# Kernel tuning notes

Measured on AMD Instinct MI355X. Metric: run time of the kernel, lower is better.

## Reference

```python
import jax, jax.numpy as jnp
import numpy as np
import math

B, S, H = 2, 2048, 1024
NH, HD = 16, 64
MAX_SCALE = 4


def setup_inputs() -> dict:
    key = jax.random.key(0)
    ks = jax.random.split(key, 8)
    s = 0.02
    return {
        "x": jax.random.normal(ks[0], (B, S, H), dtype=jnp.float32),
        "Wqkv": jax.random.normal(ks[1], (H, 3 * H), dtype=jnp.float32) * s,
        "bqkv": jnp.zeros((3 * H,), dtype=jnp.float32),
        "Wout": jax.random.normal(ks[2], (H, H), dtype=jnp.float32) * s,
        "bout": jnp.zeros((H,), dtype=jnp.float32),
        "Wscale": jax.random.normal(ks[3], (H, MAX_SCALE), dtype=jnp.float32) * s,
        "bscale": jnp.zeros((MAX_SCALE,), dtype=jnp.float32),
    }


def reference(x, Wqkv, bqkv, Wout, bout, Wscale, bscale):
    b, s, h = x.shape
    inv_sqrt_hd = 1.0 / math.sqrt(HD)
    # qkv projection -> [3, b, nh, s, hd]
    qkv = (x @ Wqkv + bqkv).reshape(b, s, 3, NH, HD).transpose(2, 0, 3, 1, 4)
    q, k, v = qkv[0], qkv[1], qkv[2]
    # per-token soft weights over scales [b, s, max_scale]
    scale_weights = jax.nn.softmax(x @ Wscale + bscale, axis=-1)
    out = jnp.zeros((b, NH, s, HD), dtype=x.dtype)
    for scale_idx in range(MAX_SCALE):
        dilation = 2 ** scale_idx
        kd = k[:, :, ::dilation]  # strided (dilated) gather of keys
        vd = v[:, :, ::dilation]
        scores = jnp.einsum("bhqd,bhkd->bhqk", q, kd) * inv_sqrt_hd
        attn = jax.nn.softmax(scores, axis=-1)
        o = jnp.einsum("bhqk,bhkd->bhqd", attn, vd)
        w = scale_weights[:, :, scale_idx][:, None, :, None]  # [b,1,s,1]
        out = out + o * w
    out = out.transpose(0, 2, 1, 3).reshape(b, s, h)
    return out @ Wout + bout
```

## Files before the change

kernel.cpp:

```cpp
#include <hip/hip_runtime.h>
#include <stdint.h>

typedef unsigned short u16;
typedef __attribute__((ext_vector_type(8))) __bf16 bf8v;
typedef __attribute__((ext_vector_type(4))) float f4v;
typedef __attribute__((ext_vector_type(16))) float f16v;

#define BB 2
#define SS 2048
#define HH 1024

#define OFF_Q   0u
#define OFF_K0  8388608u
#define OFF_K1  16777216u
#define OFF_K2  20971520u
#define OFF_K3  23068672u
#define OFF_V0  24117248u
#define OFF_V1  32505856u
#define OFF_V2  36700160u
#define OFF_V3  38797312u
#define OFF_WQT 39845888u
#define OFF_WOT 46137344u
#define OFF_XB  48234496u
#define OFF_SCW 56623104u

__device__ __forceinline__ u16 f2bf(float f) {
    union { float f; uint32_t u; } v; v.f = f;
    uint32_t r = v.u + 0x7fffu + ((v.u >> 16) & 1u);
    return (u16)(r >> 16);
}
__device__ __forceinline__ uint32_t pk2(float a, float b) {
    return (uint32_t)f2bf(a) | ((uint32_t)f2bf(b) << 16);
}
__device__ __forceinline__ uint32_t pkt2(float a, float b) {
    union { float f; uint32_t u; } x, y; x.f = a; y.f = b;
    return (x.u >> 16) | (y.u & 0xffff0000u);
}

__global__ __launch_bounds__(256) void xconv_kernel(const float* __restrict__ x,
                                                    u16* __restrict__ xb) {
    size_t t = (size_t)blockIdx.x * 256 + threadIdx.x;
    float4 v = *(const float4*)&x[t * 4];
    uint2 pk; pk.x = pk2(v.x, v.y); pk.y = pk2(v.z, v.w);
    *(uint2*)&xb[t * 4] = pk;
}

__global__ __launch_bounds__(256) void wconv_kernel(const float* __restrict__ W,
                                                    u16* __restrict__ Wt,
                                                    int N, int K) {
    __shared__ float tile[64][69];
    const int tid = threadIdx.x;
    const int n0 = blockIdx.x * 64, k0 = blockIdx.y * 64;
    const int r = tid >> 4, c4 = (tid & 15) * 4;
#pragma unroll
    for (int it = 0; it < 4; it++) {
        float4 v = *(const float4*)&W[(size_t)(k0 + it * 16 + r) * N + n0 + c4];
        tile[it * 16 + r][c4 + 0] = v.x; tile[it * 16 + r][c4 + 1] = v.y;
        tile[it * 16 + r][c4 + 2] = v.z; tile[it * 16 + r][c4 + 3] = v.w;
    }
    __syncthreads();
#pragma unroll
    for (int it = 0; it < 4; it++) {
        int n = it * 16 + r;
        uint2 pk;
        pk.x = pk2(tile[c4 + 0][n], tile[c4 + 1][n]);
        pk.y = pk2(tile[c4 + 2][n], tile[c4 + 3][n]);
        *(uint2*)&Wt[(size_t)(n0 + n) * K + k0 + c4] = pk;
    }
}

__global__ __launch_bounds__(256) void scale_kernel(const float* __restrict__ x,
                                                    const float* __restrict__ Wscale,
                                                    const float* __restrict__ bscale,
                                                    float* __restrict__ scw) {
    const int lane = threadIdx.x & 63;
    const int wid  = threadIdx.x >> 6;
    const int row  = blockIdx.x * 4 + wid;
    float a0 = 0.f, a1 = 0.f, a2 = 0.f, a3 = 0.f;
    for (int i = 0; i < 16; i++) {
        int hh = lane + i * 64;
        float xs = x[(size_t)row * HH + hh];
        float4 wv = *(const float4*)&Wscale[hh * 4];
        a0 += xs * wv.x; a1 += xs * wv.y; a2 += xs * wv.z; a3 += xs * wv.w;
    }
    for (int off = 1; off < 64; off <<= 1) {
        a0 += __shfl_xor(a0, off); a1 += __shfl_xor(a1, off);
        a2 += __shfl_xor(a2, off); a3 += __shfl_xor(a3, off);
    }
    if (lane == 0) {
        a0 += bscale[0]; a1 += bscale[1]; a2 += bscale[2]; a3 += bscale[3];
        float mx = fmaxf(fmaxf(a0, a1), fmaxf(a2, a3));
        float e0 = __expf(a0 - mx), e1 = __expf(a1 - mx);
        float e2 = __expf(a2 - mx), e3 = __expf(a3 - mx);
        float inv = 1.f / (e0 + e1 + e2 + e3);
        float4 o = {e0 * inv, e1 * inv, e2 * inv, e3 * inv};
        *(float4*)&scw[(size_t)row * 4] = o;
    }
}

template<int MODE>
__global__ __launch_bounds__(256) void gemm_bt(const u16* __restrict__ A,
                                               const u16* __restrict__ Bt,
                                               const float* __restrict__ bias,
                                               void* __restrict__ Cp,
                                               int N, int K) {
    __shared__ __align__(16) u16 At[128 * 40];
    __shared__ __align__(16) u16 Btl[128 * 40];
    const int tid  = threadIdx.x;
    const int lane = tid & 63;
    const int wid  = tid >> 6;
    const int l15  = lane & 15;
    const int quad = lane >> 4;
    const int wm = wid & 1, wn = wid >> 1;
    const int m0 = blockIdx.y * 128;
    const int n0 = blockIdx.x * 128;
    const int srow = tid >> 2;
    const int sc8  = (tid & 3) * 8;

    f4v acc[4][4];
#pragma unroll
    for (int i = 0; i < 4; i++)
#pragma unroll
        for (int j = 0; j < 4; j++) acc[i][j] = (f4v){0.f, 0.f, 0.f, 0.f};

    uint4 pa0 = *(const uint4*)(A  + (size_t)(m0 + srow) * K + sc8);
    uint4 pa1 = *(const uint4*)(A  + (size_t)(m0 + srow + 64) * K + sc8);
    uint4 pb0 = *(const uint4*)(Bt + (size_t)(n0 + srow) * K + sc8);
    uint4 pb1 = *(const uint4*)(Bt + (size_t)(n0 + srow + 64) * K + sc8);

    for (int kc = 0; kc < K; kc += 32) {
        __syncthreads();
        *(uint4*)&At[srow * 40 + sc8]         = pa0;
        *(uint4*)&At[(srow + 64) * 40 + sc8]  = pa1;
        *(uint4*)&Btl[srow * 40 + sc8]        = pb0;
        *(uint4*)&Btl[(srow + 64) * 40 + sc8] = pb1;
        __syncthreads();
        if (kc + 32 < K) {
            pa0 = *(const uint4*)(A  + (size_t)(m0 + srow) * K + kc + 32 + sc8);
            pa1 = *(const uint4*)(A  + (size_t)(m0 + srow + 64) * K + kc + 32 + sc8);
            pb0 = *(const uint4*)(Bt + (size_t)(n0 + srow) * K + kc + 32 + sc8);
            pb1 = *(const uint4*)(Bt + (size_t)(n0 + srow + 64) * K + kc + 32 + sc8);
        }
        bf8v af[4], bf[4];
#pragma unroll
        for (int t = 0; t < 4; t++) {
            af[t] = *(const bf8v*)&At[(wm * 64 + t * 16 + l15) * 40 + quad * 8];
            bf[t] = *(const bf8v*)&Btl[(wn * 64 + t * 16 + l15) * 40 + quad * 8];
        }
#pragma unroll
        for (int ti = 0; ti < 4; ti++)
#pragma unroll
            for (int tj = 0; tj < 4; tj++)
                acc[ti][tj] = __builtin_amdgcn_mfma_f32_16x16x32_bf16(af[ti], bf[tj], acc[ti][tj], 0, 0, 0);
    }

    if (MODE == 0) {
#pragma unroll
        for (int ti = 0; ti < 4; ti++)
#pragma unroll
            for (int tj = 0; tj < 4; tj++)
#pragma unroll
                for (int r = 0; r < 4; r++) {
                    int m = m0 + wm * 64 + ti * 16 + quad * 4 + r;
                    int n = n0 + wn * 64 + tj * 16 + l15;
                    ((float*)Cp)[(size_t)m * N + n] = acc[ti][tj][r] + bias[n];
                }
    } else {
        char* ws = (char*)Cp;
        u16* Qd = (u16*)ws;
        u16* K0 = (u16*)(ws + OFF_K0); u16* K1 = (u16*)(ws + OFF_K1);
        u16* K2 = (u16*)(ws + OFF_K2); u16* K3 = (u16*)(ws + OFF_K3);
        u16* V0 = (u16*)(ws + OFF_V0); u16* V1 = (u16*)(ws + OFF_V1);
        u16* V2 = (u16*)(ws + OFF_V2); u16* V3 = (u16*)(ws + OFF_V3);
        const int region = n0 >> 10;
        if (region == 0) {
#pragma unroll
            for (int ti = 0; ti < 4; ti++)
#pragma unroll
                for (int tj = 0; tj < 4; tj++)
#pragma unroll
                    for (int r = 0; r < 4; r++) {
                        int m = m0 + wm * 64 + ti * 16 + quad * 4 + r;
                        int n = n0 + wn * 64 + tj * 16 + l15;
                        Qd[(size_t)m * 1024 + n] = f2bf(acc[ti][tj][r] + bias[n]);
                    }
        } else if (region == 1) {
#pragma unroll
            for (int ti = 0; ti < 4; ti++)
#pragma unroll
                for (int tj = 0; tj < 4; tj++) {
                    int n  = n0 + wn * 64 + tj * 16 + l15;
                    int nk = n - 1024;
                    int h = nk >> 6, hd = nk & 63;
#pragma unroll
                    for (int r = 0; r < 4; r++) {
                        int m = m0 + wm * 64 + ti * 16 + quad * 4 + r;
                        int bb = m >> 11, tok = m & 2047;
                        int bh = bb * 16 + h;
                        u16 bv = f2bf((acc[ti][tj][r] + bias[n]) * 0.125f);
                        K0[((size_t)bh * 2048 + tok) * 64 + hd] = bv;
                        if (!(r & 1)) K1[((size_t)bh * 1024 + (tok >> 1)) * 64 + hd] = bv;
                        if (r == 0) {
                            K2[((size_t)bh * 512 + (tok >> 2)) * 64 + hd] = bv;
                            if (!(quad & 1)) K3[((size_t)bh * 256 + (tok >> 3)) * 64 + hd] = bv;
                        }
                    }
                }
        } else {
#pragma unroll
            for (int ti = 0; ti < 4; ti++)
#pragma unroll
                for (int tj = 0; tj < 4; tj++) {
                    int n  = n0 + wn * 64 + tj * 16 + l15;
                    int nv = n - 2048;
                    int h = nv >> 6, hd = nv & 63;
                    int tokb = m0 + wm * 64 + ti * 16 + quad * 4;
                    int bb = tokb >> 11, tok = tokb & 2047;
                    int bh = bb * 16 + h;
                    float v0 = acc[ti][tj][0] + bias[n];
                    float v1 = acc[ti][tj][1] + bias[n];
                    float v2 = acc[ti][tj][2] + bias[n];
                    float v3 = acc[ti][tj][3] + bias[n];
                    u16 c0 = f2bf(v0), c1 = f2bf(v1), c2 = f2bf(v2), c3 = f2bf(v3);
                    uint2 pk;
                    pk.x = (uint32_t)c0 | ((uint32_t)c1 << 16);
                    pk.y = (uint32_t)c2 | ((uint32_t)c3 << 16);
                    *(uint2*)&V0[((size_t)bh * 64 + hd) * 2048 + tok] = pk;
                    *(uint32_t*)&V1[((size_t)bh * 64 + hd) * 1024 + (tok >> 1)] =
                        (uint32_t)c0 | ((uint32_t)c2 << 16);
                    V2[((size_t)bh * 64 + hd) * 512 + (tok >> 2)] = c0;
                    if (!(quad & 1)) V3[((size_t)bh * 64 + hd) * 256 + (tok >> 3)] = c0;
                }
        }
    }
}

__global__ void attn_kernel(const char* __restrict__ ws) {
    __shared__ __align__(16) u16 smem[14848];
    u16* Kt0 = smem;
    u16* Kt1 = smem + 2304;
    u16* Vt0 = smem + 4608;
    u16* Vt1 = smem + 7168;
    u16* Pt  = smem + 9728;

    const u16* Qd    = (const u16*)(ws + OFF_Q);
    const float* scw = (const float*)(ws + OFF_SCW);
    u16* attnb       = (u16*)(ws + OFF_Q);

    const int tid  = threadIdx.x;
    const int lane = tid & 63;
    const int wid  = tid >> 6;
    const int l31  = lane & 31;
    const int half = lane >> 5;
    const int b = blockIdx.z, h = blockIdx.y;
    const int q  = blockIdx.x * 128 + wid * 32 + l31;
    const int bh = b * 16 + h;

    const int skey = tid >> 3;
    const int shd8 = (tid & 7) * 8;
    const int svhd = tid >> 2;
    const int svk8 = (tid & 3) * 8;

    bf8v qf[4];
#pragma unroll
    for (int ks = 0; ks < 4; ks++)
        qf[ks] = *(const bf8v*)(Qd + (size_t)(b * SS + q) * 1024 + h * 64 + ks * 16 + half * 8);

    u16* Pw = Pt + wid * 1280;

    f16v ofin[2];
#pragma unroll
    for (int ht = 0; ht < 2; ht++)
#pragma unroll
        for (int r = 0; r < 16; r++) ofin[ht][r] = 0.f;

    const uint32_t koff[4] = {OFF_K0, OFF_K1, OFF_K2, OFF_K3};
    const uint32_t voff[4] = {OFF_V0, OFF_V1, OFF_V2, OFF_V3};

    for (int s = 0; s < 4; s++) {
        const int Ss = SS >> s;
        const int nch = Ss >> 5;
        const u16* Kb = (const u16*)(ws + koff[s]) + (size_t)bh * Ss * 64;
        const u16* Vb = (const u16*)(ws + voff[s]) + (size_t)bh * 64 * Ss;

        f16v oacc[2];
#pragma unroll
        for (int ht = 0; ht < 2; ht++)
#pragma unroll
            for (int r = 0; r < 16; r++) oacc[ht][r] = 0.f;
        float ls = 0.f;

        uint4 kr = *(const uint4*)(Kb + (size_t)skey * 64 + shd8);
        uint4 vr = *(const uint4*)(Vb + (size_t)svhd * Ss + svk8);
        *(uint4*)&Kt0[skey * 72 + shd8] = kr;
        *(uint4*)&Vt0[svhd * 40 + svk8] = vr;
        if (nch > 1) {
            kr = *(const uint4*)(Kb + (size_t)(32 + skey) * 64 + shd8);
            vr = *(const uint4*)(Vb + (size_t)svhd * Ss + 32 + svk8);
        }
        __syncthreads();

        for (int c = 0; c < nch; c++) {
            u16* Ktc = (c & 1) ? Kt1 : Kt0;
            u16* Vtc = (c & 1) ? Vt1 : Vt0;
            u16* Ktn = (c & 1) ? Kt0 : Kt1;
            u16* Vtn = (c & 1) ? Vt0 : Vt1;
            f16v sa;
#pragma unroll
            for (int r = 0; r < 16; r++) sa[r] = 0.f;
#pragma unroll
            for (int ks = 0; ks < 4; ks++) {
                bf8v ka = *(const bf8v*)&Ktc[l31 * 72 + ks * 16 + half * 8];
                sa = __builtin_amdgcn_mfma_f32_32x32x16_bf16(ka, qf[ks], sa, 0, 0, 0);
            }
#pragma unroll
            for (int g = 0; g < 4; g++) {
                float e0 = __expf(sa[g * 4 + 0]);
                float e1 = __expf(sa[g * 4 + 1]);
                float e2 = __expf(sa[g * 4 + 2]);
                float e3 = __expf(sa[g * 4 + 3]);
                ls += (e0 + e1) + (e2 + e3);
                uint2 pk;
                pk.x = pkt2(e0, e1);
                pk.y = pkt2(e2, e3);
                *(uint2*)&Pw[l31 * 40 + g * 8 + half * 4] = pk;
            }
            if (c + 1 < nch) {
                *(uint4*)&Ktn[skey * 72 + shd8] = kr;
                *(uint4*)&Vtn[svhd * 40 + svk8] = vr;
            }
            if (c + 2 < nch) {
                kr = *(const uint4*)(Kb + (size_t)((c + 2) * 32 + skey) * 64 + shd8);
                vr = *(const uint4*)(Vb + (size_t)svhd * Ss + (c + 2) * 32 + svk8);
            }
            __asm__ volatile("s_waitcnt lgkmcnt(0)" ::: "memory");
#pragma unroll
            for (int kst = 0; kst < 2; kst++) {
                bf8v pb = *(const bf8v*)&Pw[l31 * 40 + kst * 16 + half * 8];
#pragma unroll
                for (int ht = 0; ht < 2; ht++) {
                    bf8v va = *(const bf8v*)&Vtc[(ht * 32 + l31) * 40 + kst * 16 + half * 8];
                    oacc[ht] = __builtin_amdgcn_mfma_f32_32x32x16_bf16(va, pb, oacc[ht], 0, 0, 0);
                }
            }
            __syncthreads();
        }
        ls += __shfl_xor(ls, 32);
        float w = scw[(size_t)(b * SS + q) * 4 + s] / ls;
#pragma unroll
        for (int ht = 0; ht < 2; ht++)
#pragma unroll
            for (int r = 0; r < 16; r++) ofin[ht][r] += w * oacc[ht][r];
    }
    const size_t base = (size_t)(b * SS + q) * 1024 + h * 64;
#pragma unroll
    for (int ht = 0; ht < 2; ht++)
#pragma unroll
        for (int g = 0; g < 4; g++) {
            uint2 pk;
            pk.x = pk2(ofin[ht][g * 4 + 0], ofin[ht][g * 4 + 1]);
            pk.y = pk2(ofin[ht][g * 4 + 2], ofin[ht][g * 4 + 3]);
            *(uint2*)&attnb[base + ht * 32 + g * 8 + half * 4] = pk;
        }
}

extern "C" void kernel_launch(void* const* d_in, const int* in_sizes, int n_in,
                              void* d_out, int out_size, void* d_ws, size_t ws_size,
                              hipStream_t stream) {
    const float* x      = (const float*)d_in[0];
    const float* Wqkv   = (const float*)d_in[1];
    const float* bqkv   = (const float*)d_in[2];
    const float* Wout   = (const float*)d_in[3];
    const float* bout   = (const float*)d_in[4];
    const float* Wscale = (const float*)d_in[5];
    const float* bscale = (const float*)d_in[6];
    float* out = (float*)d_out;

    char* ws = (char*)d_ws;
    u16*   wqt   = (u16*)(ws + OFF_WQT);
    u16*   wot   = (u16*)(ws + OFF_WOT);
    u16*   xb    = (u16*)(ws + OFF_XB);
    u16*   attnb = (u16*)(ws + OFF_Q);
    float* scw   = (float*)(ws + OFF_SCW);

    xconv_kernel<<<dim3(4096), dim3(256), 0, stream>>>(x, xb);
    wconv_kernel<<<dim3(48, 16), dim3(256), 0, stream>>>(Wqkv, wqt, 3072, 1024);
    wconv_kernel<<<dim3(16, 16), dim3(256), 0, stream>>>(Wout, wot, 1024, 1024);
    scale_kernel<<<dim3(1024), dim3(256), 0, stream>>>(x, Wscale, bscale, scw);
    gemm_bt<1><<<dim3(24, 32), dim3(256), 0, stream>>>(xb, wqt, bqkv, (void*)ws, 3072, 1024);
    attn_kernel<<<dim3(16, 16, 2), dim3(256), 0, stream>>>(ws);
    gemm_bt<0><<<dim3(8, 32), dim3(256), 0, stream>>>(attnb, wot, bout, (void*)out, 1024, 1024);
}
```

Measured before the change: 268.9 us.

## Split attention scales across two block groups and sum partials in output GEMM

When the workspace is large enough, the attention grid doubles. One block group computes only scale 0 (full-length keys) and the other computes scales 1-3, which together hold 1792 keys against 2048, so the two halves are roughly balanced. Each group writes a bf16 partial output to its own buffer, and the output projection GEMM adds the two partials while loading its A tile. This doubles the parallelism of the attention kernel (512 to 1024 blocks) to fill more CUs. In exchange, the second partial buffer must be written and read back, and the extra bf16 rounding of the partials could cost some accuracy.

```diff
diff --git a/kernel.cpp b/kernel.cpp
--- a/kernel.cpp
+++ b/kernel.cpp
@@ -23,6 +23,8 @@
 #define OFF_WOT 46137344u
 #define OFF_XB  48234496u
 #define OFF_SCW 56623104u
+#define OFF_P1  56688640u
+#define WS_SPLIT_NEED 65077248u
 
 __device__ __forceinline__ u16 f2bf(float f) {
     union { float f; uint32_t u; } v; v.f = f;
@@ -35,6 +37,11 @@
 __device__ __forceinline__ uint32_t pkt2(float a, float b) {
     union { float f; uint32_t u; } x, y; x.f = a; y.f = b;
     return (x.u >> 16) | (y.u & 0xffff0000u);
+}
+__device__ __forceinline__ uint32_t addbf2(uint32_t a, uint32_t b) {
+    float a0 = __uint_as_float(a << 16), a1 = __uint_as_float(a & 0xffff0000u);
+    float b0 = __uint_as_float(b << 16), b1 = __uint_as_float(b & 0xffff0000u);
+    return pk2(a0 + b0, a1 + b1);
 }
 
 __global__ __launch_bounds__(256) void xconv_kernel(const float* __restrict__ x,
@@ -100,6 +107,7 @@
 
 template<int MODE>
 __global__ __launch_bounds__(256) void gemm_bt(const u16* __restrict__ A,
+                                               const u16* __restrict__ A2,
                                                const u16* __restrict__ Bt,
                                                const float* __restrict__ bias,
                                                void* __restrict__ Cp,
@@ -127,11 +135,26 @@
     uint4 pa1 = *(const uint4*)(A  + (size_t)(m0 + srow + 64) * K + sc8);
     uint4 pb0 = *(const uint4*)(Bt + (size_t)(n0 + srow) * K + sc8);
     uint4 pb1 = *(const uint4*)(Bt + (size_t)(n0 + srow + 64) * K + sc8);
+    uint4 qa0, qa1;
+    if (MODE == 2) {
+        qa0 = *(const uint4*)(A2 + (size_t)(m0 + srow) * K + sc8);
+        qa1 = *(const uint4*)(A2 + (size_t)(m0 + srow + 64) * K + sc8);
+    }
 
     for (int kc = 0; kc < K; kc += 32) {
         __syncthreads();
-        *(uint4*)&At[srow * 40 + sc8]         = pa0;
-        *(uint4*)&At[(srow + 64) * 40 + sc8]  = pa1;
+        if (MODE == 2) {
+            uint4 w0, w1;
+            w0.x = addbf2(pa0.x, qa0.x); w0.y = addbf2(pa0.y, qa0.y);
+            w0.z = addbf2(pa0.z, qa0.z); w0.w = addbf2(pa0.w, qa0.w);
+            w1.x = addbf2(pa1.x, qa1.x); w1.y = addbf2(pa1.y, qa1.y);
+            w1.z = addbf2(pa1.z, qa1.z); w1.w = addbf2(pa1.w, qa1.w);
+            *(uint4*)&At[srow * 40 + sc8]        = w0;
+            *(uint4*)&At[(srow + 64) * 40 + sc8] = w1;
+        } else {
+            *(uint4*)&At[srow * 40 + sc8]        = pa0;
+            *(uint4*)&At[(srow + 64) * 40 + sc8] = pa1;
+        }
         *(uint4*)&Btl[srow * 40 + sc8]        = pb0;
         *(uint4*)&Btl[(srow + 64) * 40 + sc8] = pb1;
         __syncthreads();
@@ -140,6 +163,10 @@
             pa1 = *(const uint4*)(A  + (size_t)(m0 + srow + 64) * K + kc + 32 + sc8);
             pb0 = *(const uint4*)(Bt + (size_t)(n0 + srow) * K + kc + 32 + sc8);
             pb1 = *(const uint4*)(Bt + (size_t)(n0 + srow + 64) * K + kc + 32 + sc8);
+            if (MODE == 2) {
+                qa0 = *(const uint4*)(A2 + (size_t)(m0 + srow) * K + kc + 32 + sc8);
+                qa1 = *(const uint4*)(A2 + (size_t)(m0 + srow + 64) * K + kc + 32 + sc8);
+            }
         }
         bf8v af[4], bf[4];
 #pragma unroll
@@ -154,7 +181,7 @@
                 acc[ti][tj] = __builtin_amdgcn_mfma_f32_16x16x32_bf16(af[ti], bf[tj], acc[ti][tj], 0, 0, 0);
     }
 
-    if (MODE == 0) {
+    if (MODE != 1) {
 #pragma unroll
         for (int ti = 0; ti < 4; ti++)
 #pragma unroll
@@ -235,7 +262,7 @@
     }
 }
 
-__global__ void attn_kernel(const char* __restrict__ ws) {
+__global__ void attn_kernel(const char* __restrict__ ws, int split) {
     __shared__ __align__(16) u16 smem[14848];
     u16* Kt0 = smem;
     u16* Kt1 = smem + 2304;
@@ -245,14 +272,24 @@
 
     const u16* Qd    = (const u16*)(ws + OFF_Q);
     const float* scw = (const float*)(ws + OFF_SCW);
-    u16* attnb       = (u16*)(ws + OFF_Q);
+
+    int b, s_lo, s_hi;
+    u16* outp;
+    if (split) {
+        b = blockIdx.z >> 1;
+        if ((blockIdx.z & 1) == 0) { s_lo = 0; s_hi = 0; outp = (u16*)(ws + OFF_XB); }
+        else                       { s_lo = 1; s_hi = 3; outp = (u16*)(ws + OFF_P1); }
+    } else {
+        b = blockIdx.z; s_lo = 0; s_hi = 3;
+        outp = (u16*)(ws + OFF_Q);
+    }
 
     const int tid  = threadIdx.x;
     const int lane = tid & 63;
     const int wid  = tid >> 6;
     const int l31  = lane & 31;
     const int half = lane >> 5;
-    const int b = blockIdx.z, h = blockIdx.y;
+    const int h = blockIdx.y;
     const int q  = blockIdx.x * 128 + wid * 32 + l31;
     const int bh = b * 16 + h;
 
@@ -277,7 +314,7 @@
     const uint32_t koff[4] = {OFF_K0, OFF_K1, OFF_K2, OFF_K3};
     const uint32_t voff[4] = {OFF_V0, OFF_V1, OFF_V2, OFF_V3};
 
-    for (int s = 0; s < 4; s++) {
+    for (int s = s_lo; s <= s_hi; s++) {
         const int Ss = SS >> s;
         const int nch = Ss >> 5;
         const u16* Kb = (const u16*)(ws + koff[s]) + (size_t)bh * Ss * 64;
@@ -360,7 +397,7 @@
             uint2 pk;
             pk.x = pk2(ofin[ht][g * 4 + 0], ofin[ht][g * 4 + 1]);
             pk.y = pk2(ofin[ht][g * 4 + 2], ofin[ht][g * 4 + 3]);
-            *(uint2*)&attnb[base + ht * 32 + g * 8 + half * 4] = pk;
+            *(uint2*)&outp[base + ht * 32 + g * 8 + half * 4] = pk;
         }
 }
 
@@ -380,14 +417,22 @@
     u16*   wqt   = (u16*)(ws + OFF_WQT);
     u16*   wot   = (u16*)(ws + OFF_WOT);
     u16*   xb    = (u16*)(ws + OFF_XB);
-    u16*   attnb = (u16*)(ws + OFF_Q);
     float* scw   = (float*)(ws + OFF_SCW);
+    const int split = (ws_size >= (size_t)WS_SPLIT_NEED) ? 1 : 0;
 
     xconv_kernel<<<dim3(4096), dim3(256), 0, stream>>>(x, xb);
     wconv_kernel<<<dim3(48, 16), dim3(256), 0, stream>>>(Wqkv, wqt, 3072, 1024);
     wconv_kernel<<<dim3(16, 16), dim3(256), 0, stream>>>(Wout, wot, 1024, 1024);
     scale_kernel<<<dim3(1024), dim3(256), 0, stream>>>(x, Wscale, bscale, scw);
-    gemm_bt<1><<<dim3(24, 32), dim3(256), 0, stream>>>(xb, wqt, bqkv, (void*)ws, 3072, 1024);
-    attn_kernel<<<dim3(16, 16, 2), dim3(256), 0, stream>>>(ws);
-    gemm_bt<0><<<dim3(8, 32), dim3(256), 0, stream>>>(attnb, wot, bout, (void*)out, 1024, 1024);
-}
+    gemm_bt<1><<<dim3(24, 32), dim3(256), 0, stream>>>(
+        xb, nullptr, wqt, bqkv, (void*)ws, 3072, 1024);
+    attn_kernel<<<dim3(16, 16, split ? 4 : 2), dim3(256), 0, stream>>>(ws, split);
+    if (split) {
+        gemm_bt<2><<<dim3(8, 32), dim3(256), 0, stream>>>(
+            (const u16*)(ws + OFF_XB), (const u16*)(ws + OFF_P1), wot, bout,
+            (void*)out, 1024, 1024);
+    } else {
+        gemm_bt<0><<<dim3(8, 32), dim3(256), 0, stream>>>(
+            (const u16*)(ws + OFF_Q), nullptr, wot, bout, (void*)out, 1024, 1024);
+    }
+}
```

Measured after the change: 280.6 us. 4.4% more time.
